# Performance work log

Measured on AMD Instinct MI355X. Metric: run time of the kernel, lower is better.

Reference implementation:

```python
import jax, jax.numpy as jnp
import numpy as np

NX, NY, NZ = 128, 128, 8
N_VOX = NX * NY * NZ
V, C, HF, WF = 6, 64, 116, 200
PAD_H, PAD_W = 928.0, 1600.0  # img_pad_shape (input image after padding)
IMG_H, IMG_W = 928.0, 1600.0  # img_shape used for the valid-flag bounds check


def _make_proj_mats():
    # Structured lidar2img matrices: pinhole intrinsics + 6 yaw-distributed cameras.
    K = np.array([[500.0, 0, 400, 0], [0, 500.0, 232, 0], [0, 0, 1, 0], [0, 0, 0, 1]], dtype=np.float64)
    A = np.array([[0.0, -1, 0], [0, 0, -1], [1, 0, 0]], dtype=np.float64)  # lidar(x fwd,y left,z up)->cam(z fwd)
    mats = []
    for j in range(V):
        yaw = 2.0 * np.pi * j / V
        c, s = np.cos(yaw), np.sin(yaw)
        Rz = np.array([[c, s, 0], [-s, c, 0], [0, 0, 1]])
        T = np.eye(4)
        T[:3, :3] = A @ Rz
        T[:3, 3] = np.array([0.0, -1.0, 0.0])
        mats.append(K @ T)
    return jnp.asarray(np.stack(mats), dtype=jnp.float32)


def setup_inputs() -> dict:
    key = jax.random.key(0)
    k1, k2 = jax.random.split(key)
    x_fov = jax.random.normal(k1, (1, V, C, HF, WF), dtype=jnp.float32)
    lo = jnp.array([-50.0, -50.0, -5.0], jnp.float32)
    span = jnp.array([100.0, 100.0, 8.0], jnp.float32)
    points = jax.random.uniform(k2, (N_VOX, 3), dtype=jnp.float32) * span + lo
    proj_mats = _make_proj_mats()
    return {"x_fov": x_fov, "points": points, "proj_mats": proj_mats}


def _bilinear_sample(feat, px, py):
    # feat [C,HF,WF]; px/py [N] in feature-map pixel coords.
    # Matches F.grid_sample(mode='bilinear', padding_mode='zeros', align_corners=False).
    x0 = jnp.floor(px)
    y0 = jnp.floor(py)
    wx1 = px - x0
    wy1 = py - y0

    def gather(xi, yi, w):
        inb = (xi >= 0) & (xi < WF) & (yi >= 0) & (yi < HF)
        xc = jnp.clip(xi, 0, WF - 1).astype(jnp.int32)
        yc = jnp.clip(yi, 0, HF - 1).astype(jnp.int32)
        return feat[:, yc, xc] * (w * inb)[None, :]  # [C,N]

    return (gather(x0, y0, (1 - wx1) * (1 - wy1))
            + gather(x0 + 1, y0, wx1 * (1 - wy1))
            + gather(x0, y0 + 1, (1 - wx1) * wy1)
            + gather(x0 + 1, y0 + 1, wx1 * wy1))


def _forward(x_fov, points, proj_mats):
    n = points.shape[0]
    # points_cam2img: homogeneous projection, perspective divide
    pts_h = jnp.concatenate([points, jnp.ones((n, 1), points.dtype)], axis=-1)  # [N,4]
    cam = jnp.einsum('vij,nj->vni', proj_mats, pts_h)  # [V,N,4]
    depth = cam[..., 2]
    d_safe = jnp.where(jnp.abs(depth) > 1e-6, depth, 1e-6)
    u = cam[..., 0] / d_safe  # image-plane x in input-image pixels (scale=1, crop=0, no flip)
    v = cam[..., 1] / d_safe
    # valid_flag: in front of camera and inside img_shape
    valid = (depth > 0) & (u > 0) & (u < IMG_W) & (v > 0) & (v < IMG_H)  # [V,N]
    # normalize by img_pad_shape then map to feature-map pixels (align_corners=False)
    px = u / PAD_W * WF - 0.5
    py = v / PAD_H * HF - 0.5
    feats = jax.vmap(_bilinear_sample)(x_fov[0], px, py)  # [V,C,N]
    feats = feats * valid[:, None, :].astype(feats.dtype)
    vol = feats.sum(0)  # [C,N] masked sum over views
    cnt = valid.sum(0).astype(feats.dtype)  # [N]
    vol = jnp.where(cnt > 0, vol, 0.0) / jnp.clip(cnt, 0.001)[None, :]
    # reshape(n_voxels[::-1] + [-1]).permute(3,2,1,0) -> [C,NX,NY,NZ]
    out = jnp.transpose(vol.reshape(C, NZ, NY, NX), (0, 3, 2, 1))
    return out[None]  # [1,C,NX,NY,NZ]


def reference(x_fov, points, proj_mats):
    return _forward(x_fov, points, proj_mats)
```

## Files before the change

### kernel.cpp

```cpp
#include <hip/hip_runtime.h>
#include <hip/hip_bf16.h>
#include <hip/hip_fp16.h>

#define NXv 128
#define NYv 128
#define NZv 8
#define NVOX (NXv * NYv * NZv)
#define NV 6
#define NC 64
#define HFv 116
#define WFv 200
#define PLANE (HFv * WFv)

#define FT_BYTES ((size_t)NV * PLANE * NC * 2)

__device__ inline unsigned short f2bf(float f) {
  unsigned int x = __float_as_uint(f);
  unsigned int r = x + 0x7fffu + ((x >> 16) & 1u);
  return (unsigned short)(r >> 16);
}
__device__ inline float bf_lo(unsigned int q) { return __uint_as_float(q << 16); }
__device__ inline float bf_hi(unsigned int q) { return __uint_as_float(q & 0xffff0000u); }

__device__ inline unsigned short f2h_bits(float f) {
  __half h = __float2half(f);
  return *reinterpret_cast<unsigned short*>(&h);
}
__device__ inline float h_bits2f(unsigned short u) {
  __half_raw r; r.x = u;
  __half h = *reinterpret_cast<__half*>(&r);
  return __half2float(h);
}

__global__ __launch_bounds__(256) void transpose_feat_bf16(
    const float* __restrict__ in, unsigned int* __restrict__ out32) {
  __shared__ float tile[64][65];
  const int v  = blockIdx.y;
  const int p0 = blockIdx.x * 64;
  const float* src = in + (size_t)v * NC * PLANE;
  unsigned int* dst = out32 + (size_t)v * PLANE * (NC / 2);
  const int t = threadIdx.x;

#pragma unroll
  for (int i = 0; i < 4; ++i) {
    const int idx = i * 256 + t;
    const int c  = idx >> 4;
    const int p4 = idx & 15;
    const int pp = p0 + p4 * 4;
    if (pp < PLANE) {
      const float4 f = *(const float4*)(src + (size_t)c * PLANE + pp);
      tile[p4 * 4 + 0][c] = f.x;
      tile[p4 * 4 + 1][c] = f.y;
      tile[p4 * 4 + 2][c] = f.z;
      tile[p4 * 4 + 3][c] = f.w;
    }
  }
  __syncthreads();

#pragma unroll
  for (int i = 0; i < 4; ++i) {
    const int idx = i * 256 + t;
    const int p   = idx >> 4;
    const int c4  = idx & 15;
    const int pp  = p0 + p;
    if (pp < PLANE) {
      uint2 w;
      w.x = (unsigned int)f2bf(tile[p][c4 * 4 + 0]) |
            ((unsigned int)f2bf(tile[p][c4 * 4 + 1]) << 16);
      w.y = (unsigned int)f2bf(tile[p][c4 * 4 + 2]) |
            ((unsigned int)f2bf(tile[p][c4 * 4 + 3]) << 16);
      *(uint2*)(dst + (size_t)pp * 32 + c4 * 2) = w;
    }
  }
}

__global__ __launch_bounds__(256) void gather_fused(
    const uint4* __restrict__ feat4,
    const float* __restrict__ points,
    const float* __restrict__ proj,
    float* __restrict__ out) {
  __shared__ float tile[64][65];
  __shared__ uint4 pdl[64 * NV];
  __shared__ float invl[64];
  __shared__ float projl[96];

  const int b    = blockIdx.x;
  const int ix   = b & 127;
  const int iy0g = (b >> 7) << 3;
  const int t    = threadIdx.x;
  const int lane = t & 63;
  const int wave = t >> 6;

  if (t < 96) projl[t] = proj[t];
  if (t < 64) invl[t] = 0.0f;
  __syncthreads();

  for (int task = t; task < 64 * NV; task += 256) {
    const int slot = task / NV;
    const int v    = task - slot * NV;
    const int j    = slot >> 3;
    const int iz   = slot & 7;
    const int n    = iz * (NXv * NYv) + (iy0g + j) * NXv + ix;

    const float x = points[n * 3 + 0];
    const float y = points[n * 3 + 1];
    const float z = points[n * 3 + 2];

    const float* M = projl + v * 16;
    const float cx = M[0] * x + M[1] * y + M[2]  * z + M[3];
    const float cy = M[4] * x + M[5] * y + M[6]  * z + M[7];
    const float cz = M[8] * x + M[9] * y + M[10] * z + M[11];

    const float dz = (fabsf(cz) > 1e-6f) ? cz : 1e-6f;
    const float u  = cx / dz;
    const float vv = cy / dz;

    const bool valid = (cz > 0.0f) && (u > 0.0f) && (u < 1600.0f) &&
                       (vv > 0.0f) && (vv < 928.0f);
    if (valid) atomicAdd(&invl[slot], 1.0f);

    const float px = u  / 1600.0f * 200.0f - 0.5f;
    const float py = vv / 928.0f  * 116.0f - 0.5f;
    const float fx0 = floorf(px);
    const float fy0 = floorf(py);
    const float wx1 = px - fx0;
    const float wy1 = py - fy0;
    const float wx0 = 1.0f - wx1;
    const float wy0 = 1.0f - wy1;
    const int ix0 = (int)fx0;
    const int iy0 = (int)fy0;

    unsigned int pix[4];
    unsigned short wh[4];
    const int   xs[4] = {ix0, ix0 + 1, ix0,     ix0 + 1};
    const int   ys[4] = {iy0, iy0,     iy0 + 1, iy0 + 1};
    const float ww[4] = {wx0 * wy0, wx1 * wy0, wx0 * wy1, wx1 * wy1};
#pragma unroll
    for (int k = 0; k < 4; ++k) {
      const int xi = xs[k], yi = ys[k];
      const bool inb = (xi >= 0) && (xi < WFv) && (yi >= 0) && (yi < HFv);
      const int xc = min(max(xi, 0), WFv - 1);
      const int yc = min(max(yi, 0), HFv - 1);
      pix[k] = (unsigned int)(yc * WFv + xc);
      wh[k]  = f2h_bits((inb && valid) ? ww[k] : 0.0f);
    }

    uint4 rec;
    rec.x = pix[0] | (valid ? 0x8000u : 0u) | (pix[1] << 16);
    rec.y = pix[2] | (pix[3] << 16);
    rec.z = (unsigned int)wh[0] | ((unsigned int)wh[1] << 16);
    rec.w = (unsigned int)wh[2] | ((unsigned int)wh[3] << 16);
    pdl[slot * NV + v] = rec;
  }
  __syncthreads();
  if (t < 64) { const float c = invl[t]; invl[t] = (c > 0.0f) ? 1.0f / c : 0.0f; }
  __syncthreads();

  const int pg = lane >> 3;
  const int ch = lane & 7;

#pragma unroll
  for (int it = 0; it < 2; ++it) {
    const int sl = wave * 16 + it * 8 + pg;
    float acc[8];
#pragma unroll
    for (int j2 = 0; j2 < 8; ++j2) acc[j2] = 0.0f;

#pragma unroll
    for (int v = 0; v < NV; ++v) {
      const uint4 rec = pdl[sl * NV + v];
      if (rec.x & 0x8000u) {
        const unsigned int p00 = rec.x & 0x7fffu;
        const unsigned int p10 = rec.x >> 16;
        const unsigned int p01 = rec.y & 0xffffu;
        const unsigned int p11 = rec.y >> 16;
        const float w0 = h_bits2f((unsigned short)(rec.z & 0xffffu));
        const float w1 = h_bits2f((unsigned short)(rec.z >> 16));
        const float w2 = h_bits2f((unsigned short)(rec.w & 0xffffu));
        const float w3 = h_bits2f((unsigned short)(rec.w >> 16));

        const uint4* fb = feat4 + (size_t)v * PLANE * 8 + ch;
        const uint4 q0 = fb[(size_t)p00 * 8];
        const uint4 q1 = fb[(size_t)p10 * 8];
        const uint4 q2 = fb[(size_t)p01 * 8];
        const uint4 q3 = fb[(size_t)p11 * 8];

        acc[0] = fmaf(w0, bf_lo(q0.x), acc[0]); acc[1] = fmaf(w0, bf_hi(q0.x), acc[1]);
        acc[2] = fmaf(w0, bf_lo(q0.y), acc[2]); acc[3] = fmaf(w0, bf_hi(q0.y), acc[3]);
        acc[4] = fmaf(w0, bf_lo(q0.z), acc[4]); acc[5] = fmaf(w0, bf_hi(q0.z), acc[5]);
        acc[6] = fmaf(w0, bf_lo(q0.w), acc[6]); acc[7] = fmaf(w0, bf_hi(q0.w), acc[7]);

        acc[0] = fmaf(w1, bf_lo(q1.x), acc[0]); acc[1] = fmaf(w1, bf_hi(q1.x), acc[1]);
        acc[2] = fmaf(w1, bf_lo(q1.y), acc[2]); acc[3] = fmaf(w1, bf_hi(q1.y), acc[3]);
        acc[4] = fmaf(w1, bf_lo(q1.z), acc[4]); acc[5] = fmaf(w1, bf_hi(q1.z), acc[5]);
        acc[6] = fmaf(w1, bf_lo(q1.w), acc[6]); acc[7] = fmaf(w1, bf_hi(q1.w), acc[7]);

        acc[0] = fmaf(w2, bf_lo(q2.x), acc[0]); acc[1] = fmaf(w2, bf_hi(q2.x), acc[1]);
        acc[2] = fmaf(w2, bf_lo(q2.y), acc[2]); acc[3] = fmaf(w2, bf_hi(q2.y), acc[3]);
        acc[4] = fmaf(w2, bf_lo(q2.z), acc[4]); acc[5] = fmaf(w2, bf_hi(q2.z), acc[5]);
        acc[6] = fmaf(w2, bf_lo(q2.w), acc[6]); acc[7] = fmaf(w2, bf_hi(q2.w), acc[7]);

        acc[0] = fmaf(w3, bf_lo(q3.x), acc[0]); acc[1] = fmaf(w3, bf_hi(q3.x), acc[1]);
        acc[2] = fmaf(w3, bf_lo(q3.y), acc[2]); acc[3] = fmaf(w3, bf_hi(q3.y), acc[3]);
        acc[4] = fmaf(w3, bf_lo(q3.z), acc[4]); acc[5] = fmaf(w3, bf_hi(q3.z), acc[5]);
        acc[6] = fmaf(w3, bf_lo(q3.w), acc[6]); acc[7] = fmaf(w3, bf_hi(q3.w), acc[7]);
      }
    }

    const float inv = invl[sl];
#pragma unroll
    for (int j2 = 0; j2 < 8; ++j2) tile[sl][ch * 8 + j2] = acc[j2] * inv;
  }

  __syncthreads();

  const size_t obase = (size_t)ix * (NYv * NZv) + (size_t)iy0g * NZv + lane;
#pragma unroll
  for (int i = 0; i < 16; ++i) {
    const int c = i * 4 + wave;
    out[(size_t)c * NVOX + obase] = tile[lane][c];
  }
}

__global__ __launch_bounds__(256) void sample_fallback(
    const float* __restrict__ feat,
    const float* __restrict__ points,
    const float* __restrict__ proj,
    float* __restrict__ out) {
  const int wave = threadIdx.x >> 6;
  const int lane = threadIdx.x & 63;
  const int n = blockIdx.x * 4 + wave;

  const float x = points[n * 3 + 0];
  const float y = points[n * 3 + 1];
  const float z = points[n * 3 + 2];

  float acc = 0.0f;
  int cnt = 0;

#pragma unroll
  for (int v = 0; v < NV; ++v) {
    const float* M = proj + v * 16;
    const float cx = M[0] * x + M[1] * y + M[2]  * z + M[3];
    const float cy = M[4] * x + M[5] * y + M[6]  * z + M[7];
    const float cz = M[8] * x + M[9] * y + M[10] * z + M[11];
    const float dz = (fabsf(cz) > 1e-6f) ? cz : 1e-6f;
    const float u  = cx / dz;
    const float vv = cy / dz;
    const bool valid = (cz > 0.0f) && (u > 0.0f) && (u < 1600.0f) &&
                       (vv > 0.0f) && (vv < 928.0f);
    if (!valid) continue;
    cnt++;
    const float px = u  / 1600.0f * 200.0f - 0.5f;
    const float py = vv / 928.0f  * 116.0f - 0.5f;
    const float fx0 = floorf(px);
    const float fy0 = floorf(py);
    const float wx1 = px - fx0;
    const float wy1 = py - fy0;
    const float wx0 = 1.0f - wx1;
    const float wy0 = 1.0f - wy1;
    const int ix0 = (int)fx0;
    const int iy0 = (int)fy0;
    const float w00 = wx0 * wy0, w10 = wx1 * wy0, w01 = wx0 * wy1, w11 = wx1 * wy1;
    const float* basev = feat + ((size_t)v * NC + lane) * PLANE;
    auto tap = [&](int xi, int yi, float w) {
      if (xi >= 0 && xi < WFv && yi >= 0 && yi < HFv)
        acc += w * basev[yi * WFv + xi];
    };
    tap(ix0,     iy0,     w00);
    tap(ix0 + 1, iy0,     w10);
    tap(ix0,     iy0 + 1, w01);
    tap(ix0 + 1, iy0 + 1, w11);
  }

  const float scale = (cnt > 0) ? (1.0f / (float)cnt) : 0.0f;
  const int iz  = n >> 14;
  const int rem = n & 16383;
  const int iy  = rem >> 7;
  const int ixx = rem & 127;
  out[(((size_t)lane * NXv + ixx) * NYv + iy) * NZv + iz] = acc * scale;
}

extern "C" void kernel_launch(void* const* d_in, const int* in_sizes, int n_in,
                              void* d_out, int out_size, void* d_ws, size_t ws_size,
                              hipStream_t stream) {
  const float* x_fov  = (const float*)d_in[0];
  const float* points = (const float*)d_in[1];
  const float* proj   = (const float*)d_in[2];
  float* out = (float*)d_out;

  if (ws_size >= FT_BYTES) {
    unsigned int* ft = (unsigned int*)d_ws;
    dim3 tgrid((PLANE + 63) / 64, NV);
    transpose_feat_bf16<<<tgrid, 256, 0, stream>>>(x_fov, ft);
    gather_fused<<<NXv * NYv / 8, 256, 0, stream>>>((const uint4*)ft, points, proj, out);
  } else {
    sample_fallback<<<NVOX / 4, 256, 0, stream>>>(x_fov, points, proj, out);
  }
}
```

Baseline: 109.4 us.

## Compact valid views per voxel, remap blocks per XCD, shrink LDS tile

```diff
diff --git a/kernel.cpp b/kernel.cpp
--- a/kernel.cpp
+++ b/kernel.cpp
@@ -14,10 +14,10 @@
 
 #define FT_BYTES ((size_t)NV * PLANE * NC * 2)
 
-__device__ inline unsigned short f2bf(float f) {
+__device__ inline unsigned int f2bf(float f) {
   unsigned int x = __float_as_uint(f);
   unsigned int r = x + 0x7fffu + ((x >> 16) & 1u);
-  return (unsigned short)(r >> 16);
+  return (r >> 16) & 0xffffu;
 }
 __device__ inline float bf_lo(unsigned int q) { return __uint_as_float(q << 16); }
 __device__ inline float bf_hi(unsigned int q) { return __uint_as_float(q & 0xffff0000u); }
@@ -58,41 +58,48 @@
   __syncthreads();
 
 #pragma unroll
-  for (int i = 0; i < 4; ++i) {
+  for (int i = 0; i < 2; ++i) {
     const int idx = i * 256 + t;
-    const int p   = idx >> 4;
-    const int c4  = idx & 15;
+    const int p   = idx >> 3;
+    const int c8  = idx & 7;
     const int pp  = p0 + p;
     if (pp < PLANE) {
-      uint2 w;
-      w.x = (unsigned int)f2bf(tile[p][c4 * 4 + 0]) |
-            ((unsigned int)f2bf(tile[p][c4 * 4 + 1]) << 16);
-      w.y = (unsigned int)f2bf(tile[p][c4 * 4 + 2]) |
-            ((unsigned int)f2bf(tile[p][c4 * 4 + 3]) << 16);
-      *(uint2*)(dst + (size_t)pp * 32 + c4 * 2) = w;
-    }
-  }
-}
-
-__global__ __launch_bounds__(256) void gather_fused(
+      uint4 w;
+      w.x = f2bf(tile[p][c8 * 8 + 0]) | (f2bf(tile[p][c8 * 8 + 1]) << 16);
+      w.y = f2bf(tile[p][c8 * 8 + 2]) | (f2bf(tile[p][c8 * 8 + 3]) << 16);
+      w.z = f2bf(tile[p][c8 * 8 + 4]) | (f2bf(tile[p][c8 * 8 + 5]) << 16);
+      w.w = f2bf(tile[p][c8 * 8 + 6]) | (f2bf(tile[p][c8 * 8 + 7]) << 16);
+      *(uint4*)(dst + (size_t)pp * 32 + c8 * 4) = w;
+    }
+  }
+}
+
+__global__ __launch_bounds__(256, 8) void gather_fused(
     const uint4* __restrict__ feat4,
     const float* __restrict__ points,
     const float* __restrict__ proj,
     float* __restrict__ out) {
-  __shared__ float tile[64][65];
+  __shared__ unsigned short tile_h[64][66];
   __shared__ uint4 pdl[64 * NV];
+  __shared__ int   cntl[64];
   __shared__ float invl[64];
   __shared__ float projl[96];
 
-  const int b    = blockIdx.x;
-  const int ix   = b & 127;
-  const int iy0g = (b >> 7) << 3;
+  const int bi   = blockIdx.x;
+  const int xcd  = bi & 7;
+  const int r    = bi >> 3;
+  const int tid  = xcd * 2 + (r >> 7);
+  const int q    = r & 127;
+  const int ix   = (tid & 3) * 32 + (q & 31);
+  const int iyg  = (tid >> 2) * 4 + (q >> 5);
+  const int iy0g = iyg * 8;
+
   const int t    = threadIdx.x;
   const int lane = t & 63;
   const int wave = t >> 6;
 
   if (t < 96) projl[t] = proj[t];
-  if (t < 64) invl[t] = 0.0f;
+  if (t < 64) cntl[t] = 0;
   __syncthreads();
 
   for (int task = t; task < 64 * NV; task += 256) {
@@ -117,43 +124,46 @@
 
     const bool valid = (cz > 0.0f) && (u > 0.0f) && (u < 1600.0f) &&
                        (vv > 0.0f) && (vv < 928.0f);
-    if (valid) atomicAdd(&invl[slot], 1.0f);
-
-    const float px = u  / 1600.0f * 200.0f - 0.5f;
-    const float py = vv / 928.0f  * 116.0f - 0.5f;
-    const float fx0 = floorf(px);
-    const float fy0 = floorf(py);
-    const float wx1 = px - fx0;
-    const float wy1 = py - fy0;
-    const float wx0 = 1.0f - wx1;
-    const float wy0 = 1.0f - wy1;
-    const int ix0 = (int)fx0;
-    const int iy0 = (int)fy0;
-
-    unsigned int pix[4];
-    unsigned short wh[4];
-    const int   xs[4] = {ix0, ix0 + 1, ix0,     ix0 + 1};
-    const int   ys[4] = {iy0, iy0,     iy0 + 1, iy0 + 1};
-    const float ww[4] = {wx0 * wy0, wx1 * wy0, wx0 * wy1, wx1 * wy1};
-#pragma unroll
-    for (int k = 0; k < 4; ++k) {
-      const int xi = xs[k], yi = ys[k];
-      const bool inb = (xi >= 0) && (xi < WFv) && (yi >= 0) && (yi < HFv);
-      const int xc = min(max(xi, 0), WFv - 1);
-      const int yc = min(max(yi, 0), HFv - 1);
-      pix[k] = (unsigned int)(yc * WFv + xc);
-      wh[k]  = f2h_bits((inb && valid) ? ww[k] : 0.0f);
-    }
-
-    uint4 rec;
-    rec.x = pix[0] | (valid ? 0x8000u : 0u) | (pix[1] << 16);
-    rec.y = pix[2] | (pix[3] << 16);
-    rec.z = (unsigned int)wh[0] | ((unsigned int)wh[1] << 16);
-    rec.w = (unsigned int)wh[2] | ((unsigned int)wh[3] << 16);
-    pdl[slot * NV + v] = rec;
-  }
-  __syncthreads();
-  if (t < 64) { const float c = invl[t]; invl[t] = (c > 0.0f) ? 1.0f / c : 0.0f; }
+    if (valid) {
+      const float px = u  / 1600.0f * 200.0f - 0.5f;
+      const float py = vv / 928.0f  * 116.0f - 0.5f;
+      const float fx0 = floorf(px);
+      const float fy0 = floorf(py);
+      const float wx1 = px - fx0;
+      const float wy1 = py - fy0;
+      const float wx0 = 1.0f - wx1;
+      const float wy0 = 1.0f - wy1;
+      const int ix0 = (int)fx0;
+      const int iy0 = (int)fy0;
+
+      const bool bx0 = (ix0 >= 0) && (ix0 < WFv);
+      const bool bx1 = (ix0 + 1 >= 0) && (ix0 + 1 < WFv);
+      const bool by0 = (iy0 >= 0) && (iy0 < HFv);
+      const bool by1 = (iy0 + 1 >= 0) && (iy0 + 1 < HFv);
+
+      const int xc0 = min(max(ix0, 0), WFv - 1);
+      const int xc1 = min(max(ix0 + 1, 0), WFv - 1);
+      const int yc0 = min(max(iy0, 0), HFv - 1);
+      const int yc1 = min(max(iy0 + 1, 0), HFv - 1);
+      const unsigned int p00 = (unsigned int)(yc0 * WFv + xc0);
+      const unsigned int p10 = (unsigned int)(yc0 * WFv + xc1);
+      const unsigned int p01 = (unsigned int)(yc1 * WFv + xc0);
+      const unsigned int p11 = (unsigned int)(yc1 * WFv + xc1);
+      const unsigned int uv = (unsigned int)v;
+
+      uint4 rec;
+      rec.x = p00 | ((uv & 1u) << 15) | (p10 << 16) | (((uv >> 1) & 1u) << 31);
+      rec.y = p01 | (((uv >> 2) & 1u) << 15) | (p11 << 16);
+      rec.z = (unsigned int)f2h_bits((bx0 && by0) ? wx0 * wy0 : 0.0f) |
+              ((unsigned int)f2h_bits((bx1 && by0) ? wx1 * wy0 : 0.0f) << 16);
+      rec.w = (unsigned int)f2h_bits((bx0 && by1) ? wx0 * wy1 : 0.0f) |
+              ((unsigned int)f2h_bits((bx1 && by1) ? wx1 * wy1 : 0.0f) << 16);
+      const int idx = atomicAdd(&cntl[slot], 1);
+      pdl[slot * NV + idx] = rec;
+    }
+  }
+  __syncthreads();
+  if (t < 64) { const int c = cntl[t]; invl[t] = (c > 0) ? 1.0f / (float)c : 0.0f; }
   __syncthreads();
 
   const int pg = lane >> 3;
@@ -162,18 +172,25 @@
 #pragma unroll
   for (int it = 0; it < 2; ++it) {
     const int sl = wave * 16 + it * 8 + pg;
+    const int mycnt = cntl[sl];
+    int km = mycnt;
+    km = max(km, __shfl_xor(km, 8));
+    km = max(km, __shfl_xor(km, 16));
+    km = max(km, __shfl_xor(km, 32));
+
     float acc[8];
 #pragma unroll
     for (int j2 = 0; j2 < 8; ++j2) acc[j2] = 0.0f;
 
-#pragma unroll
-    for (int v = 0; v < NV; ++v) {
-      const uint4 rec = pdl[sl * NV + v];
-      if (rec.x & 0x8000u) {
+    for (int k = 0; k < km; ++k) {
+      if (k < mycnt) {
+        const uint4 rec = pdl[sl * NV + k];
         const unsigned int p00 = rec.x & 0x7fffu;
-        const unsigned int p10 = rec.x >> 16;
-        const unsigned int p01 = rec.y & 0xffffu;
-        const unsigned int p11 = rec.y >> 16;
+        const unsigned int p10 = (rec.x >> 16) & 0x7fffu;
+        const unsigned int p01 = rec.y & 0x7fffu;
+        const unsigned int p11 = (rec.y >> 16) & 0x7fffu;
+        const unsigned int v = ((rec.x >> 15) & 1u) | (((rec.x >> 31) & 1u) << 1) |
+                               (((rec.y >> 15) & 1u) << 2);
         const float w0 = h_bits2f((unsigned short)(rec.z & 0xffffu));
         const float w1 = h_bits2f((unsigned short)(rec.z >> 16));
         const float w2 = h_bits2f((unsigned short)(rec.w & 0xffffu));
@@ -209,7 +226,12 @@
 
     const float inv = invl[sl];
 #pragma unroll
-    for (int j2 = 0; j2 < 8; ++j2) tile[sl][ch * 8 + j2] = acc[j2] * inv;
+    for (int j2 = 0; j2 < 4; ++j2) {
+      const unsigned int pk =
+          (unsigned int)f2h_bits(acc[j2 * 2 + 0] * inv) |
+          ((unsigned int)f2h_bits(acc[j2 * 2 + 1] * inv) << 16);
+      *(unsigned int*)&tile_h[sl][ch * 8 + j2 * 2] = pk;
+    }
   }
 
   __syncthreads();
@@ -218,7 +240,8 @@
 #pragma unroll
   for (int i = 0; i < 16; ++i) {
     const int c = i * 4 + wave;
-    out[(size_t)c * NVOX + obase] = tile[lane][c];
+    const float val = h_bits2f(tile_h[lane][c]);
+    __builtin_nontemporal_store(val, &out[(size_t)c * NVOX + obase]);
   }
 }
 
```

After: 99.87 us. 1.1x faster.
